# Optimization experiments

Measured on AMD Instinct MI355X. Metric: run time of the kernel, lower is better.

## Reference

```python
import jax, jax.numpy as jnp
import numpy as np
import math

B, H, S, D = 2, 16, 2048, 64

def setup_inputs() -> dict:
    key = jax.random.key(0)
    kq, kk, kv, km = jax.random.split(key, 4)
    return {
        "query": jax.random.normal(kq, (B, H, S, D), dtype=jnp.float32),
        "key": jax.random.normal(kk, (B, H, S, D), dtype=jnp.float32),
        "value": jax.random.normal(kv, (B, H, S, D), dtype=jnp.float32),
        "mask": jax.random.randint(km, (B, 1, S, S), 0, 2, dtype=jnp.int32),
    }

def reference(query, key, value, mask):
    d = query.shape[-1]
    # scores: [B, H, S, S]
    scores = jnp.einsum("bhqd,bhkd->bhqk", query, key) / math.sqrt(d)
    masking_value = -1e9 if scores.dtype == jnp.float32 else -1e4
    scores = jnp.where(mask == 0, jnp.asarray(masking_value, scores.dtype), scores)
    p_attn = jax.nn.softmax(scores, axis=-1)
    out = jnp.einsum("bhqk,bhkd->bhqd", p_attn, value)
    return (out, p_attn)
```

## Files before the change

kernel.cpp:

```cpp
#include <hip/hip_runtime.h>

#define B_ 2
#define H_ 16
#define S_ 2048
#define D_ 64

typedef short v8s __attribute__((ext_vector_type(8)));
typedef float v4f __attribute__((ext_vector_type(4)));
typedef unsigned short u16;
typedef unsigned int   u32;
typedef unsigned long long u64;

__device__ __forceinline__ u32 pk2(float a, float b) {
    u32 ua = __float_as_uint(a) + 0x8000u;
    u32 ub = __float_as_uint(b) + 0x8000u;
    return __builtin_amdgcn_perm(ub, ua, 0x07060302u);
}

__device__ __forceinline__ v8s cvt8(const float* __restrict__ p, float s) {
    float4 x = ((const float4*)p)[0];
    float4 y = ((const float4*)p)[1];
    union { u32 u[4]; v8s v; } r;
    r.u[0] = pk2(x.x * s, x.y * s);
    r.u[1] = pk2(x.z * s, x.w * s);
    r.u[2] = pk2(y.x * s, y.y * s);
    r.u[3] = pk2(y.z * s, y.w * s);
    return r.v;
}

__device__ __forceinline__ void gll16(const void* g, void* l) {
    __builtin_amdgcn_global_load_lds(
        (const __attribute__((address_space(1))) u32*)g,
        (__attribute__((address_space(3))) u32*)l, 16, 0, 0);
}


__global__ void cvt_bf16_k(const float* __restrict__ src, u16* __restrict__ dst) {
    size_t i = (size_t)blockIdx.x * blockDim.x + threadIdx.x;
    const float* p = src + i * 8;
    float4 a = ((const float4*)p)[0], b = ((const float4*)p)[1];
    uint4 o;
    o.x = pk2(a.x, a.y); o.y = pk2(a.z, a.w);
    o.z = pk2(b.x, b.y); o.w = pk2(b.z, b.w);
    ((uint4*)dst)[i] = o;
}

__global__ void vtrans_k(const float* __restrict__ V, u16* __restrict__ Vt) {
    __shared__ u16 t[64][66];
    const int bh = blockIdx.y, s0 = blockIdx.x * 64;
    const int tid = threadIdx.x;
    {
        const int r = tid >> 2, c0 = (tid & 3) * 16;
        const float* p = V + ((size_t)bh * S_ + s0 + r) * D_ + c0;
        float4 f0 = ((const float4*)p)[0], f1 = ((const float4*)p)[1];
        float4 f2 = ((const float4*)p)[2], f3 = ((const float4*)p)[3];
        u32* tw = (u32*)&t[r][c0];
        tw[0] = pk2(f0.x, f0.y); tw[1] = pk2(f0.z, f0.w);
        tw[2] = pk2(f1.x, f1.y); tw[3] = pk2(f1.z, f1.w);
        tw[4] = pk2(f2.x, f2.y); tw[5] = pk2(f2.z, f2.w);
        tw[6] = pk2(f3.x, f3.y); tw[7] = pk2(f3.z, f3.w);
    }
    __syncthreads();
    {
        const int d = tid >> 2, t2 = tid & 3;
        const int G = t2 >> 1, hh = t2 & 1;
        const int e0 = G * 32 + hh * 8;
        u32 o[8];
        #pragma unroll
        for (int u = 0; u < 8; ++u)
            o[u] = (u32)t[e0 + u][d] | ((u32)t[e0 + 16 + u][d] << 16);
        u16* q = Vt + ((size_t)bh * D_ + d) * S_ + s0 + G * 32 + hh * 16;
        ((uint4*)q)[0] = make_uint4(o[0], o[1], o[2], o[3]);
        ((uint4*)q)[1] = make_uint4(o[4], o[5], o[6], o[7]);
    }
}

__global__ void mbits_k(const int* __restrict__ mask, u64* __restrict__ mb) {
    size_t i = (size_t)blockIdx.x * blockDim.x + threadIdx.x;
    u64 bal = __ballot(mask[i] != 0);
    if ((threadIdx.x & 63) == 0) mb[i >> 6] = bal;
}

__global__ __launch_bounds__(256, 4)
void attn_fast(const float* __restrict__ Q, const u16* __restrict__ Kb,
               const u16* __restrict__ Vt, const u32* __restrict__ mbits,
               float* __restrict__ out, float* __restrict__ P)
{
    __shared__ __align__(16) char LS[32768];
    __shared__ __align__(16) u16 pbuf[4][640];

    const int tid = threadIdx.x;
    const int w = tid >> 6, lane = tid & 63;
    const int n = lane & 15, g = lane >> 4;

    const int x = blockIdx.x;
    const int xcd = x & 7, kk = x >> 3;
    const int bh = xcd * 4 + (kk >> 5);
    const int qb = kk & 31;
    const int b = bh >> 4;
    const int q0 = qb * 64 + w * 16;

    const float* qrow = Q + ((size_t)bh * S_ + q0 + n) * D_;
    const v8s aq0 = cvt8(qrow + g * 8, 0.125f);
    const v8s aq1 = cvt8(qrow + 32 + g * 8, 0.125f);

    const int srow = 16 * w + (lane >> 3);
    const int swz16 = (((lane & 7) ^ (srow & 7)) << 4);
    const char* kB  = (const char*)(Kb + (size_t)bh * S_ * D_) + (size_t)srow * 128 + swz16;
    const char* vB  = (const char*)(Vt + (size_t)bh * D_ * S_) + (size_t)srow * 4096 + swz16;
    const char* kBA = (const char*)(Kb + (size_t)bh * S_ * D_)
                      + (size_t)(32 * w + (lane >> 3)) * 128 + swz16;

    const int C = n * 128 + (((g) ^ (n & 7)) << 4);

    const u32* mrow = mbits + ((size_t)b * S_ + q0 + g * 4) * 64;

    v4f sum = {0.f, 0.f, 0.f, 0.f};
    {
        #pragma unroll
        for (int c = 0; c < 4; ++c)
            gll16(kBA + c * 1024, LS + (size_t)w * 4096 + c * 1024);
        uint4 mnx[4];
        #pragma unroll
        for (int i = 0; i < 4; ++i) mnx[i] = *(const uint4*)(mrow + i * 64);
        __syncthreads();

        for (int T = 0; T < 16; ++T) {
            const char* KA = LS + (T & 1) * 16384;
            if (T < 15) {
                const char* src = kBA + (size_t)(T + 1) * 16384;
                char* dst = LS + ((T + 1) & 1) * 16384 + (size_t)w * 4096;
                #pragma unroll
                for (int c = 0; c < 4; ++c) gll16(src + c * 1024, dst + c * 1024);
            }
            uint4 mc[4];
            #pragma unroll
            for (int i = 0; i < 4; ++i) mc[i] = mnx[i];
            if (T < 15) {
                #pragma unroll
                for (int i = 0; i < 4; ++i)
                    mnx[i] = *(const uint4*)(mrow + i * 64 + (T + 1) * 4);
            }
            v4f acc[8];
            __builtin_amdgcn_s_setprio(1);
            #pragma unroll
            for (int s = 0; s < 8; ++s) {
                v8s kf0 = *(const v8s*)(KA + s * 2048 + C);
                v8s kf1 = *(const v8s*)(KA + s * 2048 + (C ^ 64));
                v4f z = {0.f, 0.f, 0.f, 0.f};
                z = __builtin_amdgcn_mfma_f32_16x16x32_bf16(aq0, kf0, z, 0, 0, 0);
                acc[s] = __builtin_amdgcn_mfma_f32_16x16x32_bf16(aq1, kf1, z, 0, 0, 0);
            }
            __builtin_amdgcn_s_setprio(0);
            #pragma unroll
            for (int s = 0; s < 8; ++s) {
                #pragma unroll
                for (int i = 0; i < 4; ++i) {
                    u32 wrd = (s >> 1) == 0 ? mc[i].x : (s >> 1) == 1 ? mc[i].y
                            : (s >> 1) == 2 ? mc[i].z : mc[i].w;
                    float e = ((wrd >> ((s & 1) * 16 + n)) & 1) ? __expf(acc[s][i]) : 0.f;
                    sum[i] += e;
                }
            }
            __syncthreads();
        }
    }
    #pragma unroll
    for (int i = 0; i < 4; ++i) {
        float s2 = sum[i];
        s2 += __shfl_xor(s2, 1, 64);
        s2 += __shfl_xor(s2, 2, 64);
        s2 += __shfl_xor(s2, 4, 64);
        s2 += __shfl_xor(s2, 8, 64);
        sum[i] = 1.0f / s2;
    }

    float* pb = P + ((size_t)bh * S_ + q0 + g * 4) * S_ + n;
    char* ldsw = (char*)&pbuf[w][0];
    v4f o0 = {0.f, 0.f, 0.f, 0.f}, o1 = o0, o2 = o0, o3 = o0;
    {
        #pragma unroll
        for (int c = 0; c < 2; ++c) {
            gll16(kB + (size_t)c * 1024,  LS + (size_t)w * 2048 + c * 1024);
            gll16(vB + (size_t)c * 32768, LS + 8192 + (size_t)w * 2048 + c * 1024);
        }
        uint2 mnx[4];
        #pragma unroll
        for (int i = 0; i < 4; ++i) mnx[i] = *(const uint2*)(mrow + i * 64);
        __syncthreads();

        for (int t = 0; t < 32; ++t) {
            const char* Kc = LS + (t & 1) * 16384;
            const char* Vc = Kc + 8192;
            if (t < 31) {
                char* dstb = LS + ((t + 1) & 1) * 16384;
                const char* ks = kB + (size_t)(t + 1) * 8192;
                const char* vs = vB + (size_t)(t + 1) * 128;
                #pragma unroll
                for (int c = 0; c < 2; ++c) {
                    gll16(ks + (size_t)c * 1024,  dstb + (size_t)w * 2048 + c * 1024);
                    gll16(vs + (size_t)c * 32768, dstb + 8192 + (size_t)w * 2048 + c * 1024);
                }
            }
            uint2 mc[4];
            #pragma unroll
            for (int i = 0; i < 4; ++i) mc[i] = mnx[i];
            if (t < 31) {
                #pragma unroll
                for (int i = 0; i < 4; ++i)
                    mnx[i] = *(const uint2*)(mrow + i * 64 + (t + 1) * 2);
            }
            v4f a[4];
            __builtin_amdgcn_s_setprio(1);
            #pragma unroll
            for (int s = 0; s < 4; ++s) {
                v8s kf0 = *(const v8s*)(Kc + s * 2048 + C);
                v8s kf1 = *(const v8s*)(Kc + s * 2048 + (C ^ 64));
                v4f z = {0.f, 0.f, 0.f, 0.f};
                z = __builtin_amdgcn_mfma_f32_16x16x32_bf16(aq0, kf0, z, 0, 0, 0);
                a[s] = __builtin_amdgcn_mfma_f32_16x16x32_bf16(aq1, kf1, z, 0, 0, 0);
            }
            __builtin_amdgcn_s_setprio(0);
            float* pt = pb + (size_t)t * 64;
            #pragma unroll
            for (int kg = 0; kg < 2; ++kg) {
                #pragma unroll
                for (int i = 0; i < 4; ++i) {
                    u32 wrd = kg ? mc[i].y : mc[i].x;
                    float p0 = ((wrd >> n) & 1)        ? __expf(a[2 * kg][i])     * sum[i] : 0.f;
                    float p1 = ((wrd >> (n + 16)) & 1) ? __expf(a[2 * kg + 1][i]) * sum[i] : 0.f;
                    pt[(size_t)i * S_ + kg * 32]      = p0;
                    pt[(size_t)i * S_ + kg * 32 + 16] = p1;
                    *(u32*)(ldsw + (g * 4 + i) * 80 + n * 4) = pk2(p0, p1);
                }
                v8s ap = *(const v8s*)(ldsw + n * 80 + g * 16);
                __builtin_amdgcn_s_setprio(1);
                v8s vf0 = *(const v8s*)(Vc + 0 * 2048 + (C ^ (kg << 6)));
                v8s vf1 = *(const v8s*)(Vc + 1 * 2048 + (C ^ (kg << 6)));
                v8s vf2 = *(const v8s*)(Vc + 2 * 2048 + (C ^ (kg << 6)));
                v8s vf3 = *(const v8s*)(Vc + 3 * 2048 + (C ^ (kg << 6)));
                o0 = __builtin_amdgcn_mfma_f32_16x16x32_bf16(ap, vf0, o0, 0, 0, 0);
                o1 = __builtin_amdgcn_mfma_f32_16x16x32_bf16(ap, vf1, o1, 0, 0, 0);
                o2 = __builtin_amdgcn_mfma_f32_16x16x32_bf16(ap, vf2, o2, 0, 0, 0);
                o3 = __builtin_amdgcn_mfma_f32_16x16x32_bf16(ap, vf3, o3, 0, 0, 0);
                __builtin_amdgcn_s_setprio(0);
            }
            __syncthreads();
        }
    }

    float* obase = out + ((size_t)bh * S_ + q0 + g * 4) * D_ + n;
    #pragma unroll
    for (int i = 0; i < 4; ++i) {
        obase[(size_t)i * D_]      = o0[i];
        obase[(size_t)i * D_ + 16] = o1[i];
        obase[(size_t)i * D_ + 32] = o2[i];
        obase[(size_t)i * D_ + 48] = o3[i];
    }
}

__global__ __launch_bounds__(256, 4)
void attn_fb(const float* __restrict__ Q, const float* __restrict__ K,
             const float* __restrict__ V, const int* __restrict__ mask,
             float* __restrict__ out, float* __restrict__ P)
{
    __shared__ u16 ldsbuf[4][640];
    const int tid = threadIdx.x;
    const int w = tid >> 6, lane = tid & 63;
    const int n = lane & 15, g = lane >> 4;
    const int qb = blockIdx.x, h = blockIdx.y, b = blockIdx.z;
    const int bh = b * H_ + h;
    const int q0 = qb * 64 + w * 16;

    const float* qrow = Q + ((size_t)bh * S_ + q0 + n) * D_;
    const v8s aq0 = cvt8(qrow + g * 8, 0.125f);
    const v8s aq1 = cvt8(qrow + 32 + g * 8, 0.125f);

    const int* mrow = mask + ((size_t)b * S_ + q0 + g * 4) * S_ + n;
    const float* kfbase = K + ((size_t)bh * S_ + n) * D_ + g * 8;

    auto loadK = [&](int key0, int dh) -> v8s {
        return cvt8(kfbase + (size_t)key0 * D_ + dh * 32, 1.0f);
    };
    auto loadM = [&](int i, int k0) -> u32 {
        u32 r = 0;
        if (mrow[(size_t)i * S_ + k0]) r |= 1u << n;
        if (mrow[(size_t)i * S_ + k0 + 16]) r |= 1u << (n + 16);
        return r;
    };
    auto loadV = [&](int k0, int dt) -> v8s {
        union { u32 u[4]; v8s v; } r;
        const float* vp = V + ((size_t)bh * S_ + k0 + g * 4) * D_ + dt * 16 + n;
        #pragma unroll
        for (int p2 = 0; p2 < 4; ++p2) {
            float fa = vp[(size_t)p2 * D_];
            float fb = vp[(size_t)(16 + p2) * D_];
            r.u[p2] = pk2(fa, fb);
        }
        return r.v;
    };

    v4f sum = {0.f, 0.f, 0.f, 0.f};
    for (int k0 = 0; k0 < S_; k0 += 32) {
        v4f a0 = {0.f, 0.f, 0.f, 0.f}, a1 = {0.f, 0.f, 0.f, 0.f};
        a0 = __builtin_amdgcn_mfma_f32_16x16x32_bf16(aq0, loadK(k0, 0), a0, 0, 0, 0);
        a0 = __builtin_amdgcn_mfma_f32_16x16x32_bf16(aq1, loadK(k0, 1), a0, 0, 0, 0);
        a1 = __builtin_amdgcn_mfma_f32_16x16x32_bf16(aq0, loadK(k0 + 16, 0), a1, 0, 0, 0);
        a1 = __builtin_amdgcn_mfma_f32_16x16x32_bf16(aq1, loadK(k0 + 16, 1), a1, 0, 0, 0);
        #pragma unroll
        for (int i = 0; i < 4; ++i) {
            u32 mw = loadM(i, k0);
            float e0 = ((mw >> n) & 1) ? __expf(a0[i]) : 0.f;
            float e1 = ((mw >> (n + 16)) & 1) ? __expf(a1[i]) : 0.f;
            sum[i] += e0 + e1;
        }
    }
    #pragma unroll
    for (int i = 0; i < 4; ++i) {
        float s = sum[i];
        s += __shfl_xor(s, 1, 64);
        s += __shfl_xor(s, 2, 64);
        s += __shfl_xor(s, 4, 64);
        s += __shfl_xor(s, 8, 64);
        sum[i] = 1.0f / s;
    }

    char* ldsw = (char*)&ldsbuf[w][0];
    float* pbase = P + ((size_t)bh * S_ + q0 + g * 4) * S_ + n;
    v4f o0 = {0.f, 0.f, 0.f, 0.f}, o1 = o0, o2 = o0, o3 = o0;

    for (int k0 = 0; k0 < S_; k0 += 32) {
        v4f a0 = {0.f, 0.f, 0.f, 0.f}, a1 = {0.f, 0.f, 0.f, 0.f};
        a0 = __builtin_amdgcn_mfma_f32_16x16x32_bf16(aq0, loadK(k0, 0), a0, 0, 0, 0);
        a0 = __builtin_amdgcn_mfma_f32_16x16x32_bf16(aq1, loadK(k0, 1), a0, 0, 0, 0);
        a1 = __builtin_amdgcn_mfma_f32_16x16x32_bf16(aq0, loadK(k0 + 16, 0), a1, 0, 0, 0);
        a1 = __builtin_amdgcn_mfma_f32_16x16x32_bf16(aq1, loadK(k0 + 16, 1), a1, 0, 0, 0);
        #pragma unroll
        for (int i = 0; i < 4; ++i) {
            u32 mw = loadM(i, k0);
            float p0 = ((mw >> n) & 1) ? __expf(a0[i]) * sum[i] : 0.f;
            float p1 = ((mw >> (n + 16)) & 1) ? __expf(a1[i]) * sum[i] : 0.f;
            pbase[(size_t)i * S_ + k0] = p0;
            pbase[(size_t)i * S_ + k0 + 16] = p1;
            *(u32*)(ldsw + (g * 4 + i) * 80 + (n >> 2) * 16 + (n & 3) * 4) = pk2(p0, p1);
        }
        v8s ap = *(const v8s*)(ldsw + n * 80 + g * 16);
        o0 = __builtin_amdgcn_mfma_f32_16x16x32_bf16(ap, loadV(k0, 0), o0, 0, 0, 0);
        o1 = __builtin_amdgcn_mfma_f32_16x16x32_bf16(ap, loadV(k0, 1), o1, 0, 0, 0);
        o2 = __builtin_amdgcn_mfma_f32_16x16x32_bf16(ap, loadV(k0, 2), o2, 0, 0, 0);
        o3 = __builtin_amdgcn_mfma_f32_16x16x32_bf16(ap, loadV(k0, 3), o3, 0, 0, 0);
    }

    float* obase = out + ((size_t)bh * S_ + q0 + g * 4) * D_ + n;
    #pragma unroll
    for (int i = 0; i < 4; ++i) {
        obase[(size_t)i * D_]      = o0[i];
        obase[(size_t)i * D_ + 16] = o1[i];
        obase[(size_t)i * D_ + 32] = o2[i];
        obase[(size_t)i * D_ + 48] = o3[i];
    }
}

extern "C" void kernel_launch(void* const* d_in, const int* in_sizes, int n_in,
                              void* d_out, int out_size, void* d_ws, size_t ws_size,
                              hipStream_t stream)
{
    (void)in_sizes; (void)n_in; (void)out_size;
    const float* Q = (const float*)d_in[0];
    const float* K = (const float*)d_in[1];
    const float* V = (const float*)d_in[2];
    const int* mask = (const int*)d_in[3];
    float* out = (float*)d_out;
    float* P = out + (size_t)B_ * H_ * S_ * D_;

    const size_t kb_b = (size_t)B_ * H_ * S_ * D_ * 2;
    const size_t vt_b = kb_b;
    const size_t mb_b = (size_t)B_ * S_ * S_ / 8;

    if (ws_size >= kb_b + vt_b + mb_b) {
        u16* Kb = (u16*)d_ws;
        u16* Vt = (u16*)((char*)d_ws + kb_b);
        u64* mb = (u64*)((char*)d_ws + kb_b + vt_b);
        cvt_bf16_k<<<(B_ * H_ * S_ * D_) / (256 * 8), 256, 0, stream>>>(K, Kb);
        vtrans_k<<<dim3(S_ / 64, B_ * H_), 256, 0, stream>>>(V, Vt);
        mbits_k<<<(B_ * S_ * S_) / 256, 256, 0, stream>>>(mask, mb);
        attn_fast<<<B_ * H_ * (S_ / 64), 256, 0, stream>>>(Q, Kb, Vt, (const u32*)mb, out, P);
    } else {
        attn_fb<<<dim3(S_ / 64, H_, B_), 256, 0, stream>>>(Q, K, V, mask, out, P);
    }
}
```

Before: 684.4 us.

## Transpose score MFMA fragments to vectorize P stores and drop LDS repack

Swapping the A/B operands of the QK^T MFMA puts one query row per lane with four consecutive keys. That lets each lane write P with 16-byte non-temporal vector stores instead of scalar strided stores. It also lets the bf16 P fragment for the PV MFMA be packed directly in registers, removing the per-wave LDS buffer round trip. Mask loads and the row-sum reduction shrink to one row per lane. The risk is that the key permutation in the packed P fragment must still match the V fragment layout.

```diff
diff --git a/kernel.cpp b/kernel.cpp
--- a/kernel.cpp
+++ b/kernel.cpp
@@ -87,7 +87,6 @@
                float* __restrict__ out, float* __restrict__ P)
 {
     __shared__ __align__(16) char LS[32768];
-    __shared__ __align__(16) u16 pbuf[4][640];
 
     const int tid = threadIdx.x;
     const int w = tid >> 6, lane = tid & 63;
@@ -113,16 +112,14 @@
 
     const int C = n * 128 + (((g) ^ (n & 7)) << 4);
 
-    const u32* mrow = mbits + ((size_t)b * S_ + q0 + g * 4) * 64;
-
-    v4f sum = {0.f, 0.f, 0.f, 0.f};
+    const u32* mroww = mbits + ((size_t)b * S_ + q0 + n) * 64;
+
+    float sum = 0.f;
     {
         #pragma unroll
         for (int c = 0; c < 4; ++c)
             gll16(kBA + c * 1024, LS + (size_t)w * 4096 + c * 1024);
-        uint4 mnx[4];
-        #pragma unroll
-        for (int i = 0; i < 4; ++i) mnx[i] = *(const uint4*)(mrow + i * 64);
+        uint4 mnx = *(const uint4*)(mroww);
         __syncthreads();
 
         for (int T = 0; T < 16; ++T) {
@@ -133,14 +130,9 @@
                 #pragma unroll
                 for (int c = 0; c < 4; ++c) gll16(src + c * 1024, dst + c * 1024);
             }
-            uint4 mc[4];
-            #pragma unroll
-            for (int i = 0; i < 4; ++i) mc[i] = mnx[i];
-            if (T < 15) {
-                #pragma unroll
-                for (int i = 0; i < 4; ++i)
-                    mnx[i] = *(const uint4*)(mrow + i * 64 + (T + 1) * 4);
-            }
+            uint4 mc = mnx;
+            if (T < 15) mnx = *(const uint4*)(mroww + (T + 1) * 4);
+
             v4f acc[8];
             __builtin_amdgcn_s_setprio(1);
             #pragma unroll
@@ -148,35 +140,31 @@
                 v8s kf0 = *(const v8s*)(KA + s * 2048 + C);
                 v8s kf1 = *(const v8s*)(KA + s * 2048 + (C ^ 64));
                 v4f z = {0.f, 0.f, 0.f, 0.f};
-                z = __builtin_amdgcn_mfma_f32_16x16x32_bf16(aq0, kf0, z, 0, 0, 0);
-                acc[s] = __builtin_amdgcn_mfma_f32_16x16x32_bf16(aq1, kf1, z, 0, 0, 0);
+                z = __builtin_amdgcn_mfma_f32_16x16x32_bf16(kf0, aq0, z, 0, 0, 0);
+                acc[s] = __builtin_amdgcn_mfma_f32_16x16x32_bf16(kf1, aq1, z, 0, 0, 0);
             }
             __builtin_amdgcn_s_setprio(0);
+            float ps0 = 0.f, ps1 = 0.f;
             #pragma unroll
             for (int s = 0; s < 8; ++s) {
+                u32 wrd = (s >> 1) == 0 ? mc.x : (s >> 1) == 1 ? mc.y
+                        : (s >> 1) == 2 ? mc.z : mc.w;
                 #pragma unroll
                 for (int i = 0; i < 4; ++i) {
-                    u32 wrd = (s >> 1) == 0 ? mc[i].x : (s >> 1) == 1 ? mc[i].y
-                            : (s >> 1) == 2 ? mc[i].z : mc[i].w;
-                    float e = ((wrd >> ((s & 1) * 16 + n)) & 1) ? __expf(acc[s][i]) : 0.f;
-                    sum[i] += e;
+                    float e = ((wrd >> ((s & 1) * 16 + 4 * g + i)) & 1)
+                              ? __expf(acc[s][i]) : 0.f;
+                    if (s & 1) ps1 += e; else ps0 += e;
                 }
             }
+            sum += ps0 + ps1;
             __syncthreads();
         }
     }
-    #pragma unroll
-    for (int i = 0; i < 4; ++i) {
-        float s2 = sum[i];
-        s2 += __shfl_xor(s2, 1, 64);
-        s2 += __shfl_xor(s2, 2, 64);
-        s2 += __shfl_xor(s2, 4, 64);
-        s2 += __shfl_xor(s2, 8, 64);
-        sum[i] = 1.0f / s2;
-    }
-
-    float* pb = P + ((size_t)bh * S_ + q0 + g * 4) * S_ + n;
-    char* ldsw = (char*)&pbuf[w][0];
+    sum += __shfl_xor(sum, 16, 64);
+    sum += __shfl_xor(sum, 32, 64);
+    const float inv = 1.0f / sum;
+
+    float* pbB = P + ((size_t)bh * S_ + q0 + n) * S_;
     v4f o0 = {0.f, 0.f, 0.f, 0.f}, o1 = o0, o2 = o0, o3 = o0;
     {
         #pragma unroll
@@ -184,9 +172,7 @@
             gll16(kB + (size_t)c * 1024,  LS + (size_t)w * 2048 + c * 1024);
             gll16(vB + (size_t)c * 32768, LS + 8192 + (size_t)w * 2048 + c * 1024);
         }
-        uint2 mnx[4];
-        #pragma unroll
-        for (int i = 0; i < 4; ++i) mnx[i] = *(const uint2*)(mrow + i * 64);
+        uint2 mnx = *(const uint2*)(mroww);
         __syncthreads();
 
         for (int t = 0; t < 32; ++t) {
@@ -202,14 +188,9 @@
                     gll16(vs + (size_t)c * 32768, dstb + 8192 + (size_t)w * 2048 + c * 1024);
                 }
             }
-            uint2 mc[4];
-            #pragma unroll
-            for (int i = 0; i < 4; ++i) mc[i] = mnx[i];
-            if (t < 31) {
-                #pragma unroll
-                for (int i = 0; i < 4; ++i)
-                    mnx[i] = *(const uint2*)(mrow + i * 64 + (t + 1) * 2);
-            }
+            uint2 mc = mnx;
+            if (t < 31) mnx = *(const uint2*)(mroww + (t + 1) * 2);
+
             v4f a[4];
             __builtin_amdgcn_s_setprio(1);
             #pragma unroll
@@ -217,45 +198,50 @@
                 v8s kf0 = *(const v8s*)(Kc + s * 2048 + C);
                 v8s kf1 = *(const v8s*)(Kc + s * 2048 + (C ^ 64));
                 v4f z = {0.f, 0.f, 0.f, 0.f};
-                z = __builtin_amdgcn_mfma_f32_16x16x32_bf16(aq0, kf0, z, 0, 0, 0);
-                a[s] = __builtin_amdgcn_mfma_f32_16x16x32_bf16(aq1, kf1, z, 0, 0, 0);
+                z = __builtin_amdgcn_mfma_f32_16x16x32_bf16(kf0, aq0, z, 0, 0, 0);
+                a[s] = __builtin_amdgcn_mfma_f32_16x16x32_bf16(kf1, aq1, z, 0, 0, 0);
             }
             __builtin_amdgcn_s_setprio(0);
-            float* pt = pb + (size_t)t * 64;
+
+            float* pt = pbB + (size_t)t * 64;
             #pragma unroll
             for (int kg = 0; kg < 2; ++kg) {
+                u32 wrd = kg ? mc.y : mc.x;
+                v4f p0, p1;
                 #pragma unroll
                 for (int i = 0; i < 4; ++i) {
-                    u32 wrd = kg ? mc[i].y : mc[i].x;
-                    float p0 = ((wrd >> n) & 1)        ? __expf(a[2 * kg][i])     * sum[i] : 0.f;
-                    float p1 = ((wrd >> (n + 16)) & 1) ? __expf(a[2 * kg + 1][i]) * sum[i] : 0.f;
-                    pt[(size_t)i * S_ + kg * 32]      = p0;
-                    pt[(size_t)i * S_ + kg * 32 + 16] = p1;
-                    *(u32*)(ldsw + (g * 4 + i) * 80 + n * 4) = pk2(p0, p1);
+                    p0[i] = ((wrd >> (4 * g + i)) & 1)
+                            ? __expf(a[2 * kg][i]) * inv : 0.f;
+                    p1[i] = ((wrd >> (16 + 4 * g + i)) & 1)
+                            ? __expf(a[2 * kg + 1][i]) * inv : 0.f;
                 }
-                v8s ap = *(const v8s*)(ldsw + n * 80 + g * 16);
+                __builtin_nontemporal_store(p0, (v4f*)(pt + kg * 32 + 4 * g));
+                __builtin_nontemporal_store(p1, (v4f*)(pt + kg * 32 + 16 + 4 * g));
+                union { u32 u[4]; v8s v; } ap;
+                #pragma unroll
+                for (int i = 0; i < 4; ++i) ap.u[i] = pk2(p0[i], p1[i]);
                 __builtin_amdgcn_s_setprio(1);
                 v8s vf0 = *(const v8s*)(Vc + 0 * 2048 + (C ^ (kg << 6)));
                 v8s vf1 = *(const v8s*)(Vc + 1 * 2048 + (C ^ (kg << 6)));
                 v8s vf2 = *(const v8s*)(Vc + 2 * 2048 + (C ^ (kg << 6)));
                 v8s vf3 = *(const v8s*)(Vc + 3 * 2048 + (C ^ (kg << 6)));
-                o0 = __builtin_amdgcn_mfma_f32_16x16x32_bf16(ap, vf0, o0, 0, 0, 0);
-                o1 = __builtin_amdgcn_mfma_f32_16x16x32_bf16(ap, vf1, o1, 0, 0, 0);
-                o2 = __builtin_amdgcn_mfma_f32_16x16x32_bf16(ap, vf2, o2, 0, 0, 0);
-                o3 = __builtin_amdgcn_mfma_f32_16x16x32_bf16(ap, vf3, o3, 0, 0, 0);
+                o0 = __builtin_amdgcn_mfma_f32_16x16x32_bf16(ap.v, vf0, o0, 0, 0, 0);
+                o1 = __builtin_amdgcn_mfma_f32_16x16x32_bf16(ap.v, vf1, o1, 0, 0, 0);
+                o2 = __builtin_amdgcn_mfma_f32_16x16x32_bf16(ap.v, vf2, o2, 0, 0, 0);
+                o3 = __builtin_amdgcn_mfma_f32_16x16x32_bf16(ap.v, vf3, o3, 0, 0, 0);
                 __builtin_amdgcn_s_setprio(0);
             }
             __syncthreads();
         }
     }
 
-    float* obase = out + ((size_t)bh * S_ + q0 + g * 4) * D_ + n;
+    float* obase = out + ((size_t)bh * S_ + q0 + 4 * g) * D_ + n;
     #pragma unroll
     for (int i = 0; i < 4; ++i) {
-        obase[(size_t)i * D_]      = o0[i];
-        obase[(size_t)i * D_ + 16] = o1[i];
-        obase[(size_t)i * D_ + 32] = o2[i];
-        obase[(size_t)i * D_ + 48] = o3[i];
+        __builtin_nontemporal_store(o0[i], obase + (size_t)i * D_);
+        __builtin_nontemporal_store(o1[i], obase + (size_t)i * D_ + 16);
+        __builtin_nontemporal_store(o2[i], obase + (size_t)i * D_ + 32);
+        __builtin_nontemporal_store(o3[i], obase + (size_t)i * D_ + 48);
     }
 }
 
```

New measurement: 687.5 us. Within noise of the previous version (+0.5%).
